# Kernel tuning notes

Measured on AMD Instinct MI355X. Metric: run time of the kernel, lower is better.

Reference implementation:

```python
import jax, jax.numpy as jnp
import numpy as np


def setup_inputs() -> dict:
    key = jax.random.key(0)
    ks = jax.random.split(key, 10)
    B, C, H = 128, 768, 12
    d = C // H
    t_h = t_w = 8
    s_h = s_w = 16
    Nt = t_h * t_w * 2          # 128 template tokens
    Ns = s_h * s_w + 4          # 260 search tokens
    N = Nt + Ns                 # 388
    s = 0.02
    return {
        "x": jax.random.normal(ks[0], (B, N, C), jnp.float32),
        "mem": jax.random.normal(ks[1], (B, H, d, d), jnp.float32),
        "z": jnp.ones((B, H, d, 1), jnp.float32),
        "qkv_w": jax.random.normal(ks[2], (3 * C, C), jnp.float32) * s,
        "qkv_b": jnp.zeros((3 * C,), jnp.float32),
        "proj_w": jax.random.normal(ks[3], (C, C), jnp.float32) * s,
        "proj_b": jnp.zeros((C,), jnp.float32),
        "memk_w": jax.random.normal(ks[4], (C, C), jnp.float32) * s,
        "memk_b": jnp.zeros((C,), jnp.float32),
        "memv_w": jax.random.normal(ks[5], (C, C), jnp.float32) * s,
        "memv_b": jnp.zeros((C,), jnp.float32),
        "betas": jax.random.normal(ks[6], (1, H, 1, d), jnp.float32),
        "t_h": t_h, "t_w": t_w, "s_h": s_h, "s_w": s_w,
    }


def reference(x, mem, z, qkv_w, qkv_b, proj_w, proj_b,
              memk_w, memk_b, memv_w, memv_b, betas,
              t_h, t_w, s_h, s_w):
    B, N, C = x.shape
    H = betas.shape[1]
    d = C // H
    Nt = t_h * t_w * 2
    Ns = s_h * s_w + 4
    scale = 1.0 / jnp.sqrt(jnp.float32(d))

    qkv = x @ qkv_w.T + qkv_b                       # [B,N,3C]
    qkv = qkv.reshape(B, N, 3, C)
    q_f, k_f, v_f = qkv[:, :, 0], qkv[:, :, 1], qkv[:, :, 2]  # [B,N,C]

    def heads(t):  # [B,N,C] -> [B,H,N,d]
        return t.reshape(B, -1, H, d).transpose(0, 2, 1, 3)

    q, k, v = heads(q_f), heads(k_f), heads(v_f)

    # memory k/v projections act on the raw (C-dim) search split of k,v
    k_s_mem = heads(k_f[:, Nt:, :] @ memk_w.T + memk_b)  # [B,H,Ns,d]
    v_s_mem = heads(v_f[:, Nt:, :] @ memv_w.T + memv_b)  # [B,H,Ns,d]

    q_mt, q_s = q[:, :, :Nt], q[:, :, Nt:]
    k_mt = k[:, :, :Nt]
    v_mt = v[:, :, :Nt]

    # template self-attention (q_mt only attends to k_mt)
    attn_mt = jax.nn.softmax(jnp.einsum('bhqd,bhkd->bhqk', q_mt, k_mt) * scale, axis=-1)
    x_mt = jnp.einsum('bhqk,bhkd->bhqd', attn_mt, v_mt)          # [B,H,Nt,d]
    x_mt = x_mt.transpose(0, 2, 1, 3).reshape(B, Nt, C)

    # search attends to full sequence
    attn_s = jax.nn.softmax(jnp.einsum('bhqd,bhkd->bhqk', q_s, k) * scale, axis=-1)
    x_s = jnp.einsum('bhqk,bhkd->bhqd', attn_s, v)               # [B,H,Ns,d]

    # linear-attention memory read (ELU feature map)
    sigma_q = jax.nn.elu(q_s) + 1.0                              # [B,H,Ns,d]
    att_mem = (sigma_q @ mem) / (sigma_q @ z)                    # [B,H,Ns,d]

    # delta-rule memory update
    sigma_k = jax.nn.elu(k_s_mem) + 1.0                          # [B,H,Ns,d]
    zz = jnp.sum(sigma_k, axis=-2, keepdims=True).swapaxes(-2, -1)  # [B,H,d,1]
    pred = (sigma_k @ mem) / (sigma_k @ z)                       # [B,H,Ns,d]
    mem_new = mem + jnp.einsum('bhnd,bhne->bhde', sigma_k, v_s_mem - pred)
    z_new = z + zz

    beta = jax.nn.sigmoid(betas)                                 # [1,H,1,d]
    x_s = beta * att_mem + (1.0 - beta) * x_s
    x_s = x_s.transpose(0, 2, 1, 3).reshape(B, Ns, C)

    out = jnp.concatenate([x_mt, x_s], axis=1) @ proj_w.T + proj_b
    return out, mem_new, z_new
```

## Files before the change

### kernel.cpp

```cpp
#include <hip/hip_runtime.h>

typedef unsigned short u16;
typedef __attribute__((ext_vector_type(8))) short  vbf8;
typedef __attribute__((ext_vector_type(4))) float  vf4;

#define B_   128
#define N_   388
#define NT   128
#define NS   260
#define C_   768
#define H_   12
#define D_   64
#define K3   2304

#define QKV_LEN  114425856ll
#define KSM_LEN  25559040ll
#define CAT_LEN  38141952ll
#define MEM_LEN  6291456ll

#define SPS  288
#define SPL  296

#define WOFF_QKV  0ll
#define WOFF_MEMK 1769472ll
#define WOFF_MEMV 2359296ll
#define WOFF_PROJ 2949120ll
#define WTOT     3538944ll
__device__ __align__(16) u16 g_wbf[3538944];

__device__ __forceinline__ float bf2f(u16 u) {
    union { unsigned int i; float f; } v; v.i = ((unsigned int)u) << 16; return v.f;
}
__device__ __forceinline__ u16 f2bf(float f) {
    union { float f; unsigned int i; } v; v.f = f;
    unsigned int r = v.i + 0x7fffu + ((v.i >> 16) & 1u);
    return (u16)(r >> 16);
}
__device__ __forceinline__ float elu1(float x) { return x > 0.f ? x + 1.f : __expf(x); }

__device__ __forceinline__ void gload_lds16(const u16* g, u16* l) {
    __builtin_amdgcn_global_load_lds(
        (const __attribute__((address_space(1))) unsigned int*)g,
        (__attribute__((address_space(3))) unsigned int*)l, 16, 0, 0);
}

__global__ __launch_bounds__(256) void convert_all(
    const float* __restrict__ x, u16* __restrict__ x_bf,
    const float* __restrict__ s0, const float* __restrict__ s1,
    const float* __restrict__ s2, const float* __restrict__ s3)
{
    int bid = blockIdx.x;
    if (bid < 2048) {
        long long i0 = ((long long)bid * 256 + threadIdx.x) * 8;
        long long stride = 2048ll * 256 * 8;
        for (long long i = i0; i < CAT_LEN; i += stride) {
            float4 a = *(const float4*)(x + i);
            float4 b = *(const float4*)(x + i + 4);
            ushort4 u1; u1.x = f2bf(a.x); u1.y = f2bf(a.y); u1.z = f2bf(a.z); u1.w = f2bf(a.w);
            ushort4 u2; u2.x = f2bf(b.x); u2.y = f2bf(b.y); u2.z = f2bf(b.z); u2.w = f2bf(b.w);
            *(ushort4*)(x_bf + i)     = u1;
            *(ushort4*)(x_bf + i + 4) = u2;
        }
    } else {
        long long i = ((long long)(bid - 2048) * 256 + threadIdx.x) * 8;
        if (i >= WTOT) return;
        const float* src; long long off;
        if (i < WOFF_MEMK)      { src = s0; off = i; }
        else if (i < WOFF_MEMV) { src = s1; off = i - WOFF_MEMK; }
        else if (i < WOFF_PROJ) { src = s2; off = i - WOFF_MEMV; }
        else                    { src = s3; off = i - WOFF_PROJ; }
        float4 a = *(const float4*)(src + off);
        float4 b = *(const float4*)(src + off + 4);
        ushort4 u1; u1.x = f2bf(a.x); u1.y = f2bf(a.y); u1.z = f2bf(a.z); u1.w = f2bf(a.w);
        ushort4 u2; u2.x = f2bf(b.x); u2.y = f2bf(b.y); u2.z = f2bf(b.z); u2.w = f2bf(b.w);
        *(ushort4*)(g_wbf + i)     = u1;
        *(ushort4*)(g_wbf + i + 4) = u2;
    }
}

__global__ __launch_bounds__(256) void memT_kernel(
    const float* __restrict__ memin, u16* __restrict__ memT)
{
    __shared__ float ml[64 * 65];
    int bh = blockIdx.x, t = threadIdx.x;
    const float* src = memin + (long long)bh * 4096;
#pragma unroll
    for (int i = 0; i < 16; i++) {
        int idx = i * 256 + t;
        ml[(idx >> 6) * 65 + (idx & 63)] = src[idx];
    }
    __syncthreads();
    u16* dst = memT + (long long)bh * 4096;
#pragma unroll
    for (int i = 0; i < 16; i++) {
        int o = i * 256 + t;
        int dout = o >> 6, din = o & 63;
        dst[o] = f2bf(ml[din * 65 + dout]);
    }
}

template<int CF32>
__device__ __forceinline__ void gemm_body(
    int wgid, int ngrid,
    const u16* __restrict__ A, long long off0, int rows_per_b,
    long long stride_b, long long stride_r,
    const u16* __restrict__ W, const float* __restrict__ bias,
    void* __restrict__ Cv, int Nout, int nbx)
{
    __shared__ __align__(16) u16 lds[2][2][4096];

    int t = threadIdx.x;

    int wg = (wgid & 7) * (ngrid >> 3) + (wgid >> 3);
    int m0 = (wg / nbx) * 128;
    int n0 = (wg % nbx) * 128;

    int lane = t & 63, w = t >> 6;
    int w512 = w * 512;

    int srow  = t >> 2;
    int scol  = (((t & 3) ^ (srow & 3))) * 8;
    long long aoff0, aoff1;
    {
        int g1 = m0 + srow, g2 = g1 + 64;
        int b1 = g1 / rows_per_b, j1 = g1 - b1 * rows_per_b;
        int b2 = g2 / rows_per_b, j2 = g2 - b2 * rows_per_b;
        aoff0 = off0 + (long long)b1 * stride_b + (long long)j1 * stride_r + scol;
        aoff1 = off0 + (long long)b2 * stride_b + (long long)j2 * stride_r + scol;
    }
    const u16* wp0 = W + (long long)(n0 + srow) * 768 + scol;
    const u16* wp1 = W + (long long)(n0 + srow + 64) * 768 + scol;

    int lr = lane & 15, kg = lane >> 4;
    int wm = w >> 1, wn = w & 1;
    int aslot = (kg ^ (lr & 3)) * 8;
    int abase = (wm * 64 + lr) * 32 + aslot;
    int bbase = (wn * 64 + lr) * 32 + aslot;

    vf4 acc[4][4];
#pragma unroll
    for (int i = 0; i < 4; i++)
#pragma unroll
        for (int j = 0; j < 4; j++) acc[i][j] = vf4{0.f, 0.f, 0.f, 0.f};

    auto stage = [&](int buf, int kt) {
        gload_lds16(A + aoff0 + kt, &lds[buf][0][w512]);
        gload_lds16(A + aoff1 + kt, &lds[buf][0][2048 + w512]);
        gload_lds16(wp0 + kt,       &lds[buf][1][w512]);
        gload_lds16(wp1 + kt,       &lds[buf][1][2048 + w512]);
    };

    stage(0, 0);
    __syncthreads();

    int cur = 0;
    for (int kt = 0; kt < 768; kt += 32) {
        if (kt != 736) stage(cur ^ 1, kt + 32);

        vbf8 af[4], bf[4];
#pragma unroll
        for (int f = 0; f < 4; f++) {
            af[f] = *(const vbf8*)&lds[cur][0][abase + f * 512];
            bf[f] = *(const vbf8*)&lds[cur][1][bbase + f * 512];
        }
#pragma unroll
        for (int i = 0; i < 4; i++)
#pragma unroll
            for (int j = 0; j < 4; j++)
                acc[i][j] = __builtin_amdgcn_mfma_f32_16x16x32_bf16(
                    af[i], bf[j], acc[i][j], 0, 0, 0);

        __syncthreads();
        cur ^= 1;
    }

    if (!CF32) {
        u16* ct = &lds[0][0][0];
#pragma unroll
        for (int i = 0; i < 4; i++)
#pragma unroll
            for (int j = 0; j < 4; j++) {
                int col = wn * 64 + j * 16 + lr;
                float bb = bias[n0 + col];
#pragma unroll
                for (int r = 0; r < 4; r++)
                    ct[(wm * 64 + i * 16 + kg * 4 + r) * 128 + col] =
                        f2bf(acc[i][j][r] + bb);
            }
        __syncthreads();
        int col0 = (t & 15) * 8;
#pragma unroll
        for (int rr = 0; rr < 8; rr++) {
            int row_l = rr * 16 + (t >> 4);
            vbf8 v = *(const vbf8*)&ct[row_l * 128 + col0];
            *(vbf8*)((u16*)Cv + (long long)(m0 + row_l) * Nout + n0 + col0) = v;
        }
    } else {
        float* cf = (float*)&lds[0][0][0];
#pragma unroll
        for (int p = 0; p < 2; p++) {
            if (wm == p) {
#pragma unroll
                for (int i = 0; i < 4; i++)
#pragma unroll
                    for (int j = 0; j < 4; j++) {
                        int col = wn * 64 + j * 16 + lr;
                        float bb = bias[n0 + col];
#pragma unroll
                        for (int r = 0; r < 4; r++)
                            cf[(i * 16 + kg * 4 + r) * 128 + col] =
                                acc[i][j][r] + bb;
                    }
            }
            __syncthreads();
            int col0 = (t & 15) * 8;
#pragma unroll
            for (int rr = 0; rr < 4; rr++) {
                int row_l = rr * 16 + (t >> 4);
                float4 v0 = *(const float4*)&cf[row_l * 128 + col0];
                float4 v1 = *(const float4*)&cf[row_l * 128 + col0 + 4];
                float* dst = (float*)Cv + (long long)(m0 + p * 64 + row_l) * Nout + n0 + col0;
                *(float4*)dst = v0;
                *(float4*)(dst + 4) = v1;
            }
            __syncthreads();
        }
    }
}

template<int CF32>
__global__ __launch_bounds__(256) void gemm_mfma(
    const u16* __restrict__ A, long long off0, int rows_per_b,
    long long stride_b, long long stride_r,
    long long w_off, const float* __restrict__ bias,
    void* __restrict__ Cv, int Nout, int nbx)
{
    gemm_body<CF32>(blockIdx.x, gridDim.x, A, off0, rows_per_b, stride_b,
                    stride_r, g_wbf + w_off, bias, Cv, Nout, nbx);
}

__global__ __launch_bounds__(256) void gemm_mfma_dual(
    const u16* __restrict__ A, long long off0a, long long off0b,
    int rows_per_b, long long stride_b, long long stride_r,
    long long w_offa, long long w_offb,
    const float* __restrict__ biasa, const float* __restrict__ biasb,
    void* __restrict__ Cva, void* __restrict__ Cvb, int Nout, int nbx, int half)
{
    int bid = blockIdx.x;
    if (bid < half)
        gemm_body<0>(bid, half, A, off0a, rows_per_b, stride_b, stride_r,
                     g_wbf + w_offa, biasa, Cva, Nout, nbx);
    else
        gemm_body<0>(bid - half, half, A, off0b, rows_per_b, stride_b, stride_r,
                     g_wbf + w_offb, biasb, Cvb, Nout, nbx);
}

#define SKP 416
#define VTS 424
__global__ __launch_bounds__(512) void attn_fused(
    const u16* __restrict__ qkv, const u16* __restrict__ memT,
    const float* __restrict__ zin, const float* __restrict__ betas,
    u16* __restrict__ concat)
{
    __shared__ __align__(16) u16 Kl[SKP * 64];
    __shared__ __align__(16) u16 Vt[64 * VTS];
    __shared__ __align__(16) u16 Pl[8][16 * 40];
    __shared__ float red[8][16];

    int bh = blockIdx.x;
    int b = bh / H_, h = bh % H_;
    int t = threadIdx.x, lane = t & 63, w = t >> 6;
    int lr = lane & 15, q4 = lane >> 4;

    {
        int key0 = t >> 3;
        int d0 = (t & 7) * 8;
        for (int kp = 0; kp < SKP; kp += 64) {
            int key = kp + key0;
            if (key < SKP) {
                vbf8 kv, vv;
#pragma unroll
                for (int u = 0; u < 8; u++) { ((short*)&kv)[u] = 0; ((short*)&vv)[u] = 0; }
                if (key < N_) {
                    const u16* base = qkv + ((long long)(b * N_ + key)) * K3 + h * D_;
                    kv = *(const vbf8*)(base + C_ + d0);
                    vv = *(const vbf8*)(base + 2 * C_ + d0);
                }
                *(vbf8*)((char*)Kl + ((key * 128 + d0 * 2) ^ ((key & 7) << 4))) = kv;
#pragma unroll
                for (int u = 0; u < 8; u++) Vt[(d0 + u) * VTS + key] = ((u16*)&vv)[u];
            }
        }
    }
    __syncthreads();

    const float* zp = zin + bh * 64;
    const u16* mtb = memT + (long long)bh * 4096;

    for (int s = w; s < 17; s += 8) {
        int qtok = NT + s * 16 + lr;
        if (qtok > N_ - 1) qtok = N_ - 1;
        const u16* qbase = qkv + ((long long)(b * N_ + qtok)) * K3 + h * D_;
        vbf8 qf0 = *(const vbf8*)(qbase + q4 * 8);
        vbf8 qf1 = *(const vbf8*)(qbase + 32 + q4 * 8);

        vbf8 qs0, qs1;
#pragma unroll
        for (int j = 0; j < 8; j++) {
            ((u16*)&qs0)[j] = f2bf(bf2f(((u16*)&qf0)[j]) * 0.125f);
            ((u16*)&qs1)[j] = f2bf(bf2f(((u16*)&qf1)[j]) * 0.125f);
        }

        vf4 S[13][2];
#pragma unroll
        for (int kt = 0; kt < 13; kt++) {
#pragma unroll
            for (int ks = 0; ks < 2; ks++) {
                int krow = kt * 32 + ks * 16 + lr;
                int swz = (krow & 7) << 4;
                vbf8 b0 = *(const vbf8*)((char*)Kl + ((krow * 128 + q4 * 16) ^ swz));
                vbf8 b1 = *(const vbf8*)((char*)Kl + ((krow * 128 + 64 + q4 * 16) ^ swz));
                vf4 z4 = vf4{0.f, 0.f, 0.f, 0.f};
                vf4 sv = __builtin_amdgcn_mfma_f32_16x16x32_bf16(qs0, b0, z4, 0, 0, 0);
                S[kt][ks] = __builtin_amdgcn_mfma_f32_16x16x32_bf16(qs1, b1, sv, 0, 0, 0);
            }
        }
#pragma unroll
        for (int ks = 0; ks < 2; ks++)
#pragma unroll
            for (int r = 0; r < 4; r++)
                if (ks * 16 + lr >= 4) S[12][ks][r] = -1e30f;

        float mx[4];
#pragma unroll
        for (int r = 0; r < 4; r++) mx[r] = S[0][0][r];
#pragma unroll
        for (int kt = 0; kt < 13; kt++)
#pragma unroll
            for (int ks = 0; ks < 2; ks++)
#pragma unroll
                for (int r = 0; r < 4; r++) mx[r] = fmaxf(mx[r], S[kt][ks][r]);
#pragma unroll
        for (int off = 1; off <= 8; off <<= 1)
#pragma unroll
            for (int r = 0; r < 4; r++) mx[r] = fmaxf(mx[r], __shfl_xor(mx[r], off));

        float l[4] = {0.f, 0.f, 0.f, 0.f};
#pragma unroll
        for (int kt = 0; kt < 13; kt++)
#pragma unroll
            for (int ks = 0; ks < 2; ks++)
#pragma unroll
                for (int r = 0; r < 4; r++) {
                    float p = __expf(S[kt][ks][r] - mx[r]);
                    S[kt][ks][r] = p;
                    l[r] += p;
                }
#pragma unroll
        for (int off = 1; off <= 8; off <<= 1)
#pragma unroll
            for (int r = 0; r < 4; r++) l[r] += __shfl_xor(l[r], off);

        vf4 accO[4];
#pragma unroll
        for (int dc = 0; dc < 4; dc++) accO[dc] = vf4{0.f, 0.f, 0.f, 0.f};
#pragma unroll
        for (int kt = 0; kt < 13; kt++) {
            u16* pw = Pl[w];
#pragma unroll
            for (int ks = 0; ks < 2; ks++)
#pragma unroll
                for (int r = 0; r < 4; r++)
                    pw[(q4 * 4 + r) * 40 + ks * 16 + lr] = f2bf(S[kt][ks][r]);
            vbf8 pf = *(const vbf8*)&Pl[w][lr * 40 + q4 * 8];
#pragma unroll
            for (int dc = 0; dc < 4; dc++) {
                vbf8 vf_ = *(const vbf8*)&Vt[(dc * 16 + lr) * VTS + kt * 32 + q4 * 8];
                accO[dc] = __builtin_amdgcn_mfma_f32_16x16x32_bf16(pf, vf_, accO[dc], 0, 0, 0);
            }
        }

        float invl[4];
#pragma unroll
        for (int r = 0; r < 4; r++) invl[r] = 1.f / l[r];

        vbf8 sq0, sq1;
        float dpart = 0.f;
#pragma unroll
        for (int j = 0; j < 8; j++) {
            float s0 = elu1(bf2f(((u16*)&qf0)[j]));
            float s1 = elu1(bf2f(((u16*)&qf1)[j]));
            ((u16*)&sq0)[j] = f2bf(s0);
            ((u16*)&sq1)[j] = f2bf(s1);
            dpart += s0 * zp[q4 * 8 + j] + s1 * zp[32 + q4 * 8 + j];
        }
        dpart += __shfl_xor(dpart, 16);
        dpart += __shfl_xor(dpart, 32);
        if (q4 == 0) red[w][lr] = dpart;

        vf4 am[4];
#pragma unroll
        for (int dc = 0; dc < 4; dc++) {
            vbf8 b0 = *(const vbf8*)(mtb + (dc * 16 + lr) * 64 + q4 * 8);
            vbf8 b1 = *(const vbf8*)(mtb + (dc * 16 + lr) * 64 + 32 + q4 * 8);
            vf4 z4 = vf4{0.f, 0.f, 0.f, 0.f};
            vf4 a = __builtin_amdgcn_mfma_f32_16x16x32_bf16(sq0, b0, z4, 0, 0, 0);
            am[dc] = __builtin_amdgcn_mfma_f32_16x16x32_bf16(sq1, b1, a, 0, 0, 0);
        }
        float den[4];
#pragma unroll
        for (int r = 0; r < 4; r++) den[r] = 1.f / red[w][q4 * 4 + r];

#pragma unroll
        for (int dc = 0; dc < 4; dc++) {
            float bb = betas[h * D_ + dc * 16 + lr];
            float beta = 1.f / (1.f + __expf(-bb));
#pragma unroll
            for (int r = 0; r < 4; r++) {
                int qs = s * 16 + q4 * 4 + r;
                if (qs < NS) {
                    float o = beta * (am[dc][r] * den[r]) +
                              (1.f - beta) * (accO[dc][r] * invl[r]);
                    concat[((long long)(b * N_ + NT + qs)) * C_ + h * D_ + dc * 16 + lr] = f2bf(o);
                }
            }
        }
    }

    if (w > 0) {
        for (int m = w - 1; m < 8; m += 7) {
            int qtok = m * 16 + lr;
            const u16* qbase = qkv + ((long long)(b * N_ + qtok)) * K3 + h * D_;
            vbf8 qf0 = *(const vbf8*)(qbase + q4 * 8);
            vbf8 qf1 = *(const vbf8*)(qbase + 32 + q4 * 8);
            vbf8 qs0, qs1;
#pragma unroll
            for (int j = 0; j < 8; j++) {
                ((u16*)&qs0)[j] = f2bf(bf2f(((u16*)&qf0)[j]) * 0.125f);
                ((u16*)&qs1)[j] = f2bf(bf2f(((u16*)&qf1)[j]) * 0.125f);
            }

            vf4 S4[4][2];
#pragma unroll
            for (int kt = 0; kt < 4; kt++) {
#pragma unroll
                for (int ks = 0; ks < 2; ks++) {
                    int krow = kt * 32 + ks * 16 + lr;
                    int swz = (krow & 7) << 4;
                    vbf8 b0 = *(const vbf8*)((char*)Kl + ((krow * 128 + q4 * 16) ^ swz));
                    vbf8 b1 = *(const vbf8*)((char*)Kl + ((krow * 128 + 64 + q4 * 16) ^ swz));
                    vf4 z4 = vf4{0.f, 0.f, 0.f, 0.f};
                    vf4 sv = __builtin_amdgcn_mfma_f32_16x16x32_bf16(qs0, b0, z4, 0, 0, 0);
                    S4[kt][ks] = __builtin_amdgcn_mfma_f32_16x16x32_bf16(qs1, b1, sv, 0, 0, 0);
                }
            }

            float mx[4];
#pragma unroll
            for (int r = 0; r < 4; r++) mx[r] = S4[0][0][r];
#pragma unroll
            for (int kt = 0; kt < 4; kt++)
#pragma unroll
                for (int ks = 0; ks < 2; ks++)
#pragma unroll
                    for (int r = 0; r < 4; r++) mx[r] = fmaxf(mx[r], S4[kt][ks][r]);
#pragma unroll
            for (int off = 1; off <= 8; off <<= 1)
#pragma unroll
                for (int r = 0; r < 4; r++) mx[r] = fmaxf(mx[r], __shfl_xor(mx[r], off));

            float l[4] = {0.f, 0.f, 0.f, 0.f};
#pragma unroll
            for (int kt = 0; kt < 4; kt++)
#pragma unroll
                for (int ks = 0; ks < 2; ks++)
#pragma unroll
                    for (int r = 0; r < 4; r++) {
                        float p = __expf(S4[kt][ks][r] - mx[r]);
                        S4[kt][ks][r] = p;
                        l[r] += p;
                    }
#pragma unroll
            for (int off = 1; off <= 8; off <<= 1)
#pragma unroll
                for (int r = 0; r < 4; r++) l[r] += __shfl_xor(l[r], off);

            vf4 accO[4];
#pragma unroll
            for (int dc = 0; dc < 4; dc++) accO[dc] = vf4{0.f, 0.f, 0.f, 0.f};
#pragma unroll
            for (int kt = 0; kt < 4; kt++) {
                u16* pw = Pl[w];
#pragma unroll
                for (int ks = 0; ks < 2; ks++)
#pragma unroll
                    for (int r = 0; r < 4; r++)
                        pw[(q4 * 4 + r) * 40 + ks * 16 + lr] = f2bf(S4[kt][ks][r]);
                vbf8 pf = *(const vbf8*)&Pl[w][lr * 40 + q4 * 8];
#pragma unroll
                for (int dc = 0; dc < 4; dc++) {
                    vbf8 vf_ = *(const vbf8*)&Vt[(dc * 16 + lr) * VTS + kt * 32 + q4 * 8];
                    accO[dc] = __builtin_amdgcn_mfma_f32_16x16x32_bf16(pf, vf_, accO[dc], 0, 0, 0);
                }
            }

            float invl[4];
#pragma unroll
            for (int r = 0; r < 4; r++) invl[r] = 1.f / l[r];

            int qt0 = m * 16;
#pragma unroll
            for (int dc = 0; dc < 4; dc++)
#pragma unroll
                for (int r = 0; r < 4; r++) {
                    int row = qt0 + q4 * 4 + r;
                    concat[((long long)(b * N_ + row)) * C_ + h * D_ + dc * 16 + lr] =
                        f2bf(accO[dc][r] * invl[r]);
                }
        }
    }
}

__global__ __launch_bounds__(512) void sigma_pred_mem(
    const u16* __restrict__ ksm, const u16* __restrict__ vsm,
    const u16* __restrict__ memT, const float* __restrict__ zin,
    const float* __restrict__ memin, float* __restrict__ mem_out,
    float* __restrict__ z_out)
{
    __shared__ __align__(16) u16 sigL[64][SPL];
    __shared__ __align__(16) u16 wL[64][SPL];
    __shared__ float red[8][16];
    __shared__ float zpart[8][64];
    __shared__ float zlds[64];

    int bh = blockIdx.x;
    int b = bh / H_, h = bh % H_;
    int t = threadIdx.x, lane = t & 63, w = t >> 6;
    int lr = lane & 15, q4 = lane >> 4;

    if (t < 64) zlds[t] = zin[bh * 64 + t];
    __syncthreads();

    const u16* mtb = memT + (long long)bh * 4096;
    float zacc[16];
#pragma unroll
    for (int j = 0; j < 16; j++) zacc[j] = 0.f;

    for (int s = w; s < 18; s += 8) {
        int n0 = s * 16;
        int nrow = n0 + lr;
        bool vrow = nrow < NS;
        int nclamp = vrow ? nrow : NS - 1;
        const u16* kbase = ksm + ((long long)(b * NS + nclamp)) * C_ + h * D_;
        vbf8 k0 = *(const vbf8*)(kbase + q4 * 8);
        vbf8 k1 = *(const vbf8*)(kbase + 32 + q4 * 8);

        vbf8 sq0, sq1;
        float dpart = 0.f;
#pragma unroll
        for (int j = 0; j < 8; j++) {
            float s0 = vrow ? elu1(bf2f(((u16*)&k0)[j])) : 0.f;
            float s1 = vrow ? elu1(bf2f(((u16*)&k1)[j])) : 0.f;
            u16 b0 = f2bf(s0), b1 = f2bf(s1);
            ((u16*)&sq0)[j] = b0;
            ((u16*)&sq1)[j] = b1;
            zacc[j]     += s0;
            zacc[8 + j] += s1;
            dpart += s0 * zlds[q4 * 8 + j] + s1 * zlds[32 + q4 * 8 + j];
            sigL[q4 * 8 + j][n0 + lr]      = b0;
            sigL[32 + q4 * 8 + j][n0 + lr] = b1;
        }
        dpart += __shfl_xor(dpart, 16);
        dpart += __shfl_xor(dpart, 32);
        if (q4 == 0) red[w][lr] = dpart;

        vf4 am[4];
#pragma unroll
        for (int dc = 0; dc < 4; dc++) {
            vbf8 b0 = *(const vbf8*)(mtb + (dc * 16 + lr) * 64 + q4 * 8);
            vbf8 b1 = *(const vbf8*)(mtb + (dc * 16 + lr) * 64 + 32 + q4 * 8);
            vf4 z4 = vf4{0.f, 0.f, 0.f, 0.f};
            vf4 a = __builtin_amdgcn_mfma_f32_16x16x32_bf16(sq0, b0, z4, 0, 0, 0);
            am[dc] = __builtin_amdgcn_mfma_f32_16x16x32_bf16(sq1, b1, a, 0, 0, 0);
        }
        float rden[4];
#pragma unroll
        for (int r = 0; r < 4; r++) rden[r] = 1.f / red[w][q4 * 4 + r];

#pragma unroll
        for (int dc = 0; dc < 4; dc++) {
            int e = dc * 16 + lr;
#pragma unroll
            for (int r = 0; r < 4; r++) {
                int nn = n0 + q4 * 4 + r;
                float wv = 0.f;
                if (nn < NS) {
                    float pv = am[dc][r] * rden[r];
                    wv = bf2f(vsm[((long long)(b * NS + nn)) * C_ + h * D_ + e]) - pv;
                }
                wL[e][n0 + q4 * 4 + r] = f2bf(wv);
            }
        }
    }

#pragma unroll
    for (int off = 1; off <= 8; off <<= 1)
#pragma unroll
        for (int j = 0; j < 16; j++) zacc[j] += __shfl_xor(zacc[j], off);
    if (lr == 0) {
#pragma unroll
        for (int j = 0; j < 8; j++) {
            zpart[w][q4 * 8 + j]      = zacc[j];
            zpart[w][32 + q4 * 8 + j] = zacc[8 + j];
        }
    }
    __syncthreads();

    if (t < 64) {
        float tot = 0.f;
#pragma unroll
        for (int ww = 0; ww < 8; ww++) tot += zpart[ww][t];
        z_out[bh * 64 + t] = zlds[t] + tot;
    }

    long long mb = (long long)bh * 4096;
#pragma unroll
    for (int p = 0; p < 2; p++) {
        int tid2 = w * 2 + p;
        int i = tid2 >> 2, j = tid2 & 3;
        vf4 acc = vf4{0.f, 0.f, 0.f, 0.f};
#pragma unroll
        for (int kt = 0; kt < SPS; kt += 32) {
            vbf8 af = *(const vbf8*)&sigL[i * 16 + lr][kt + q4 * 8];
            vbf8 bf = *(const vbf8*)&wL[j * 16 + lr][kt + q4 * 8];
            acc = __builtin_amdgcn_mfma_f32_16x16x32_bf16(af, bf, acc, 0, 0, 0);
        }
        int e = j * 16 + lr;
#pragma unroll
        for (int r = 0; r < 4; r++) {
            int dd = i * 16 + q4 * 4 + r;
            mem_out[mb + dd * 64 + e] = memin[mb + dd * 64 + e] + acc[r];
        }
    }
}

extern "C" void kernel_launch(void* const* d_in, const int* in_sizes, int n_in,
                              void* d_out, int out_size, void* d_ws, size_t ws_size,
                              hipStream_t stream)
{
    const float* x      = (const float*)d_in[0];
    const float* mem    = (const float*)d_in[1];
    const float* z      = (const float*)d_in[2];
    const float* qkv_w  = (const float*)d_in[3];
    const float* qkv_b  = (const float*)d_in[4];
    const float* proj_w = (const float*)d_in[5];
    const float* proj_b = (const float*)d_in[6];
    const float* memk_w = (const float*)d_in[7];
    const float* memk_b = (const float*)d_in[8];
    const float* memv_w = (const float*)d_in[9];
    const float* memv_b = (const float*)d_in[10];
    const float* betas  = (const float*)d_in[11];

    u16* ws     = (u16*)d_ws;
    u16* qkv    = ws;
    u16* ksm    = qkv + QKV_LEN;
    u16* vsm    = ksm + KSM_LEN;
    u16* concat = vsm + KSM_LEN;

    float* out     = (float*)d_out;
    float* mem_out = out + CAT_LEN;
    float* z_out   = mem_out + MEM_LEN;

    u16* x_bf = concat;
    u16* memT = (u16*)out;

    convert_all<<<dim3(2048 + 1728), dim3(256), 0, stream>>>(
        x, x_bf, qkv_w, memk_w, memv_w, proj_w);
    memT_kernel<<<dim3(B_ * H_), dim3(256), 0, stream>>>(mem, memT);

    gemm_mfma<0><<<dim3(6984), dim3(256), 0, stream>>>(
        x_bf, 0ll, 49664, 0ll, 768ll, WOFF_QKV, qkv_b, qkv, K3, 18);
    gemm_mfma_dual<<<dim3(3120), dim3(256), 0, stream>>>(
        qkv, (long long)(NT * K3 + C_), (long long)(NT * K3 + 2 * C_),
        NS, (long long)N_ * K3, (long long)K3,
        WOFF_MEMK, WOFF_MEMV, memk_b, memv_b, ksm, vsm, C_, 6, 1560);
    attn_fused<<<dim3(B_ * H_), dim3(512), 0, stream>>>(
        qkv, memT, z, betas, concat);
    sigma_pred_mem<<<dim3(B_ * H_), dim3(512), 0, stream>>>(
        ksm, vsm, memT, z, mem, mem_out, z_out);
    gemm_mfma<1><<<dim3(2328), dim3(256), 0, stream>>>(
        concat, 0ll, 49664, 0ll, 768ll, WOFF_PROJ, proj_b, out, C_, 6);
}
```

Measured before the change: 858.4 us.

## Fuse fp32-to-bf16 input conversion into QKV GEMM loads and use exp2 softmax

The separate pass that converts x to bf16 is removed. The QKV GEMM now reads fp32 x directly through registers, packs it to bf16, and writes it into LDS after the MFMAs, double-buffered. This drops a full read-write round trip of x, but each QKV tile now reads A twice as many bytes and loses the async global-to-LDS path for A. Separately, the softmax scale folds in log2(e) so exp2f can replace __expf.

```diff
diff --git a/kernel.cpp b/kernel.cpp
--- a/kernel.cpp
+++ b/kernel.cpp
@@ -21,6 +21,8 @@
 #define SPS  288
 #define SPL  296
 
+#define SM2  0.18033688f
+
 #define WOFF_QKV  0ll
 #define WOFF_MEMK 1769472ll
 #define WOFF_MEMV 2359296ll
@@ -44,38 +46,29 @@
         (__attribute__((address_space(3))) unsigned int*)l, 16, 0, 0);
 }
 
-__global__ __launch_bounds__(256) void convert_all(
-    const float* __restrict__ x, u16* __restrict__ x_bf,
+__device__ __forceinline__ vbf8 pack8(float4 a, float4 b) {
+    vbf8 v;
+    ((u16*)&v)[0] = f2bf(a.x); ((u16*)&v)[1] = f2bf(a.y);
+    ((u16*)&v)[2] = f2bf(a.z); ((u16*)&v)[3] = f2bf(a.w);
+    ((u16*)&v)[4] = f2bf(b.x); ((u16*)&v)[5] = f2bf(b.y);
+    ((u16*)&v)[6] = f2bf(b.z); ((u16*)&v)[7] = f2bf(b.w);
+    return v;
+}
+
+__global__ __launch_bounds__(256) void convert_weights(
     const float* __restrict__ s0, const float* __restrict__ s1,
     const float* __restrict__ s2, const float* __restrict__ s3)
 {
-    int bid = blockIdx.x;
-    if (bid < 2048) {
-        long long i0 = ((long long)bid * 256 + threadIdx.x) * 8;
-        long long stride = 2048ll * 256 * 8;
-        for (long long i = i0; i < CAT_LEN; i += stride) {
-            float4 a = *(const float4*)(x + i);
-            float4 b = *(const float4*)(x + i + 4);
-            ushort4 u1; u1.x = f2bf(a.x); u1.y = f2bf(a.y); u1.z = f2bf(a.z); u1.w = f2bf(a.w);
-            ushort4 u2; u2.x = f2bf(b.x); u2.y = f2bf(b.y); u2.z = f2bf(b.z); u2.w = f2bf(b.w);
-            *(ushort4*)(x_bf + i)     = u1;
-            *(ushort4*)(x_bf + i + 4) = u2;
-        }
-    } else {
-        long long i = ((long long)(bid - 2048) * 256 + threadIdx.x) * 8;
-        if (i >= WTOT) return;
-        const float* src; long long off;
-        if (i < WOFF_MEMK)      { src = s0; off = i; }
-        else if (i < WOFF_MEMV) { src = s1; off = i - WOFF_MEMK; }
-        else if (i < WOFF_PROJ) { src = s2; off = i - WOFF_MEMV; }
-        else                    { src = s3; off = i - WOFF_PROJ; }
-        float4 a = *(const float4*)(src + off);
-        float4 b = *(const float4*)(src + off + 4);
-        ushort4 u1; u1.x = f2bf(a.x); u1.y = f2bf(a.y); u1.z = f2bf(a.z); u1.w = f2bf(a.w);
-        ushort4 u2; u2.x = f2bf(b.x); u2.y = f2bf(b.y); u2.z = f2bf(b.z); u2.w = f2bf(b.w);
-        *(ushort4*)(g_wbf + i)     = u1;
-        *(ushort4*)(g_wbf + i + 4) = u2;
-    }
+    long long i = ((long long)blockIdx.x * 256 + threadIdx.x) * 8;
+    if (i >= WTOT) return;
+    const float* src; long long off;
+    if (i < WOFF_MEMK)      { src = s0; off = i; }
+    else if (i < WOFF_MEMV) { src = s1; off = i - WOFF_MEMK; }
+    else if (i < WOFF_PROJ) { src = s2; off = i - WOFF_MEMV; }
+    else                    { src = s3; off = i - WOFF_PROJ; }
+    float4 a = *(const float4*)(src + off);
+    float4 b = *(const float4*)(src + off + 4);
+    *(vbf8*)(g_wbf + i) = pack8(a, b);
 }
 
 __global__ __launch_bounds__(256) void memT_kernel(
@@ -99,10 +92,10 @@
     }
 }
 
-template<int CF32>
+template<int AF32, int CF32>
 __device__ __forceinline__ void gemm_body(
     int wgid, int ngrid,
-    const u16* __restrict__ A, long long off0, int rows_per_b,
+    const void* __restrict__ Av, long long off0, int rows_per_b,
     long long stride_b, long long stride_r,
     const u16* __restrict__ W, const float* __restrict__ bias,
     void* __restrict__ Cv, int Nout, int nbx)
@@ -143,19 +136,44 @@
 #pragma unroll
         for (int j = 0; j < 4; j++) acc[i][j] = vf4{0.f, 0.f, 0.f, 0.f};
 
-    auto stage = [&](int buf, int kt) {
-        gload_lds16(A + aoff0 + kt, &lds[buf][0][w512]);
-        gload_lds16(A + aoff1 + kt, &lds[buf][0][2048 + w512]);
-        gload_lds16(wp0 + kt,       &lds[buf][1][w512]);
-        gload_lds16(wp1 + kt,       &lds[buf][1][2048 + w512]);
+    const float* Af = (const float*)Av;
+    const u16*   Ab = (const u16*)Av;
+
+    auto stageW = [&](int buf, int kt) {
+        gload_lds16(wp0 + kt, &lds[buf][1][w512]);
+        gload_lds16(wp1 + kt, &lds[buf][1][2048 + w512]);
     };
 
-    stage(0, 0);
+    if (AF32) {
+        float4 a0 = *(const float4*)(Af + aoff0);
+        float4 a1 = *(const float4*)(Af + aoff0 + 4);
+        float4 a2 = *(const float4*)(Af + aoff1);
+        float4 a3 = *(const float4*)(Af + aoff1 + 4);
+        *(vbf8*)&lds[0][0][t * 8]        = pack8(a0, a1);
+        *(vbf8*)&lds[0][0][2048 + t * 8] = pack8(a2, a3);
+    } else {
+        gload_lds16(Ab + aoff0, &lds[0][0][w512]);
+        gload_lds16(Ab + aoff1, &lds[0][0][2048 + w512]);
+    }
+    stageW(0, 0);
     __syncthreads();
 
     int cur = 0;
     for (int kt = 0; kt < 768; kt += 32) {
-        if (kt != 736) stage(cur ^ 1, kt + 32);
+        bool last = (kt == 736);
+        float4 na0, na1, na2, na3;
+        if (!last) {
+            if (AF32) {
+                na0 = *(const float4*)(Af + aoff0 + kt + 32);
+                na1 = *(const float4*)(Af + aoff0 + kt + 36);
+                na2 = *(const float4*)(Af + aoff1 + kt + 32);
+                na3 = *(const float4*)(Af + aoff1 + kt + 36);
+            } else {
+                gload_lds16(Ab + aoff0 + kt + 32, &lds[cur ^ 1][0][w512]);
+                gload_lds16(Ab + aoff1 + kt + 32, &lds[cur ^ 1][0][2048 + w512]);
+            }
+            stageW(cur ^ 1, kt + 32);
+        }
 
         vbf8 af[4], bf[4];
 #pragma unroll
@@ -170,6 +188,10 @@
                 acc[i][j] = __builtin_amdgcn_mfma_f32_16x16x32_bf16(
                     af[i], bf[j], acc[i][j], 0, 0, 0);
 
+        if (!last && AF32) {
+            *(vbf8*)&lds[cur ^ 1][0][t * 8]        = pack8(na0, na1);
+            *(vbf8*)&lds[cur ^ 1][0][2048 + t * 8] = pack8(na2, na3);
+        }
         __syncthreads();
         cur ^= 1;
     }
@@ -228,15 +250,15 @@
     }
 }
 
-template<int CF32>
+template<int AF32, int CF32>
 __global__ __launch_bounds__(256) void gemm_mfma(
-    const u16* __restrict__ A, long long off0, int rows_per_b,
+    const void* __restrict__ A, long long off0, int rows_per_b,
     long long stride_b, long long stride_r,
     long long w_off, const float* __restrict__ bias,
     void* __restrict__ Cv, int Nout, int nbx)
 {
-    gemm_body<CF32>(blockIdx.x, gridDim.x, A, off0, rows_per_b, stride_b,
-                    stride_r, g_wbf + w_off, bias, Cv, Nout, nbx);
+    gemm_body<AF32, CF32>(blockIdx.x, gridDim.x, A, off0, rows_per_b, stride_b,
+                          stride_r, g_wbf + w_off, bias, Cv, Nout, nbx);
 }
 
 __global__ __launch_bounds__(256) void gemm_mfma_dual(
@@ -248,11 +270,11 @@
 {
     int bid = blockIdx.x;
     if (bid < half)
-        gemm_body<0>(bid, half, A, off0a, rows_per_b, stride_b, stride_r,
-                     g_wbf + w_offa, biasa, Cva, Nout, nbx);
+        gemm_body<0, 0>(bid, half, A, off0a, rows_per_b, stride_b, stride_r,
+                        g_wbf + w_offa, biasa, Cva, Nout, nbx);
     else
-        gemm_body<0>(bid - half, half, A, off0b, rows_per_b, stride_b, stride_r,
-                     g_wbf + w_offb, biasb, Cvb, Nout, nbx);
+        gemm_body<0, 0>(bid - half, half, A, off0b, rows_per_b, stride_b, stride_r,
+                        g_wbf + w_offb, biasb, Cvb, Nout, nbx);
 }
 
 #define SKP 416
@@ -307,8 +329,8 @@
         vbf8 qs0, qs1;
 #pragma unroll
         for (int j = 0; j < 8; j++) {
-            ((u16*)&qs0)[j] = f2bf(bf2f(((u16*)&qf0)[j]) * 0.125f);
-            ((u16*)&qs1)[j] = f2bf(bf2f(((u16*)&qf1)[j]) * 0.125f);
+            ((u16*)&qs0)[j] = f2bf(bf2f(((u16*)&qf0)[j]) * SM2);
+            ((u16*)&qs1)[j] = f2bf(bf2f(((u16*)&qf1)[j]) * SM2);
         }
 
         vf4 S[13][2];
@@ -352,7 +374,7 @@
             for (int ks = 0; ks < 2; ks++)
 #pragma unroll
                 for (int r = 0; r < 4; r++) {
-                    float p = __expf(S[kt][ks][r] - mx[r]);
+                    float p = exp2f(S[kt][ks][r] - mx[r]);
                     S[kt][ks][r] = p;
                     l[r] += p;
                 }
@@ -436,8 +458,8 @@
             vbf8 qs0, qs1;
 #pragma unroll
             for (int j = 0; j < 8; j++) {
-                ((u16*)&qs0)[j] = f2bf(bf2f(((u16*)&qf0)[j]) * 0.125f);
-                ((u16*)&qs1)[j] = f2bf(bf2f(((u16*)&qf1)[j]) * 0.125f);
+                ((u16*)&qs0)[j] = f2bf(bf2f(((u16*)&qf0)[j]) * SM2);
+                ((u16*)&qs1)[j] = f2bf(bf2f(((u16*)&qf1)[j]) * SM2);
             }
 
             vf4 S4[4][2];
@@ -476,7 +498,7 @@
                 for (int ks = 0; ks < 2; ks++)
 #pragma unroll
                     for (int r = 0; r < 4; r++) {
-                        float p = __expf(S4[kt][ks][r] - mx[r]);
+                        float p = exp2f(S4[kt][ks][r] - mx[r]);
                         S4[kt][ks][r] = p;
                         l[r] += p;
                     }
@@ -671,15 +693,13 @@
     float* mem_out = out + CAT_LEN;
     float* z_out   = mem_out + MEM_LEN;
 
-    u16* x_bf = concat;
     u16* memT = (u16*)out;
 
-    convert_all<<<dim3(2048 + 1728), dim3(256), 0, stream>>>(
-        x, x_bf, qkv_w, memk_w, memv_w, proj_w);
+    convert_weights<<<dim3(1728), dim3(256), 0, stream>>>(qkv_w, memk_w, memv_w, proj_w);
     memT_kernel<<<dim3(B_ * H_), dim3(256), 0, stream>>>(mem, memT);
 
-    gemm_mfma<0><<<dim3(6984), dim3(256), 0, stream>>>(
-        x_bf, 0ll, 49664, 0ll, 768ll, WOFF_QKV, qkv_b, qkv, K3, 18);
+    gemm_mfma<1, 0><<<dim3(6984), dim3(256), 0, stream>>>(
+        x, 0ll, 49664, 0ll, 768ll, WOFF_QKV, qkv_b, qkv, K3, 18);
     gemm_mfma_dual<<<dim3(3120), dim3(256), 0, stream>>>(
         qkv, (long long)(NT * K3 + C_), (long long)(NT * K3 + 2 * C_),
         NS, (long long)N_ * K3, (long long)K3,
@@ -688,6 +708,6 @@
         qkv, memT, z, betas, concat);
     sigma_pred_mem<<<dim3(B_ * H_), dim3(512), 0, stream>>>(
         ksm, vsm, memT, z, mem, mem_out, z_out);
-    gemm_mfma<1><<<dim3(2328), dim3(256), 0, stream>>>(
+    gemm_mfma<0, 1><<<dim3(2328), dim3(256), 0, stream>>>(
         concat, 0ll, 49664, 0ll, 768ll, WOFF_PROJ, proj_b, out, C_, 6);
 }
```

Result: slower. 886.5 us (+3.3%).
